# Performance work log

Hardware: AMD Instinct MI355X
Metric: run time of the kernel (lower is better)

The kernel has to match this reference:

```python
import jax, jax.numpy as jnp
import numpy as np
from jax import lax

B = 8; DIM = 256; NH = 8; PATCH = 8; WS = 28; STRIDE = 8; PAD = 14; ORF = 2.0; IMG = 448


def conv2d(x, w, stride, pad, groups=1):
    return lax.conv_general_dilated(
        x, w, (stride, stride), [(pad, pad), (pad, pad)],
        dimension_numbers=('NCHW', 'OIHW', 'NCHW'), feature_group_count=groups)


def ln_ch(x, g, b):
    # LayerNormProxy: LayerNorm over channel dim of NCHW
    m = jnp.mean(x, 1, keepdims=True)
    v = jnp.mean((x - m) ** 2, 1, keepdims=True)
    return (x - m) * lax.rsqrt(v + 1e-5) * g[None, :, None, None] + b[None, :, None, None]


def bilinear_sample(x, grid):
    # x: (N,C,H,W); grid: (N,Hg,Wg,2) in (x,y) order, [-1,1], align_corners=True, zeros padding
    N, C, H, W = x.shape
    gx = (grid[..., 0] + 1.0) * 0.5 * (W - 1)
    gy = (grid[..., 1] + 1.0) * 0.5 * (H - 1)
    x0 = jnp.floor(gx); y0 = jnp.floor(gy)
    x1 = x0 + 1.0; y1 = y0 + 1.0
    wx1 = gx - x0; wx0 = 1.0 - wx1
    wy1 = gy - y0; wy0 = 1.0 - wy1
    xf = x.reshape(N, C, H * W)

    def corner(ix, iy, w):
        valid = (ix >= 0) & (ix <= W - 1) & (iy >= 0) & (iy <= H - 1)
        ii = (jnp.clip(iy, 0, H - 1) * W + jnp.clip(ix, 0, W - 1)).astype(jnp.int32).reshape(N, -1)
        vals = jax.vmap(lambda f, i: f[:, i])(xf, ii)  # (N,C,Hg*Wg)
        return vals * (w * valid).reshape(N, 1, -1)

    out = (corner(x0, y0, wx0 * wy0) + corner(x1, y0, wx1 * wy0)
           + corner(x0, y1, wx0 * wy1) + corner(x1, y1, wx1 * wy1))
    return out.reshape(N, C, grid.shape[1], grid.shape[2])


def setup_inputs() -> dict:
    key = jax.random.key(0)
    ks = jax.random.split(key, 12)
    s = 0.02
    CG = 64
    return {
        'x': jax.random.normal(ks[0], (B, 3, IMG, IMG), jnp.float32),
        'patch_w': jax.random.normal(ks[1], (DIM, 3, PATCH, PATCH), jnp.float32) * s,
        'patch_b': jnp.zeros((DIM,), jnp.float32),
        'ln1_g': jnp.ones((DIM,), jnp.float32),
        'ln1_b': jnp.zeros((DIM,), jnp.float32),
        'wq': jax.random.normal(ks[2], (DIM, DIM), jnp.float32) * s,
        'bq': jnp.zeros((DIM,), jnp.float32),
        'wk': jax.random.normal(ks[3], (DIM, DIM), jnp.float32) * s,
        'bk': jnp.zeros((DIM,), jnp.float32),
        'wv': jax.random.normal(ks[4], (DIM, DIM), jnp.float32) * s,
        'bv': jnp.zeros((DIM,), jnp.float32),
        'wo': jax.random.normal(ks[5], (DIM, DIM), jnp.float32) * s,
        'bo': jnp.zeros((DIM,), jnp.float32),
        'off_dw_w': jax.random.normal(ks[6], (CG, 1, WS, WS), jnp.float32) * s,
        'off_dw_b': jnp.zeros((CG,), jnp.float32),
        'off_ln_g': jnp.ones((CG,), jnp.float32),
        'off_ln_b': jnp.zeros((CG,), jnp.float32),
        'off_pw_w': jax.random.normal(ks[7], (2, CG), jnp.float32) * s,
        'rpe_w1': jax.random.normal(ks[8], (32, 2), jnp.float32) * 0.1,
        'rpe_b1': jnp.zeros((32,), jnp.float32),
        'rpe_w2': jax.random.normal(ks[9], (2, 32), jnp.float32) * 0.1,
    }


def reference(x, patch_w, patch_b, ln1_g, ln1_b, wq, bq, wk, bk, wv, bv, wo, bo,
              off_dw_w, off_dw_b, off_ln_g, off_ln_b, off_pw_w, rpe_w1, rpe_b1, rpe_w2):
    Bn = x.shape[0]
    # patch embedding: Conv2d(3, dim, patch, patch) + LayerNormProxy
    feat = conv2d(x, patch_w, PATCH, 0) + patch_b[None, :, None, None]
    feat = ln_ch(feat, ln1_g, ln1_b)
    H, W = feat.shape[2], feat.shape[3]  # 56, 56
    G = (H // WS) * (W // WS)            # 4 groups
    CG = DIM // G; GH = NH // G; HC = DIM // NH
    # q projection (1x1 conv)
    q = jnp.einsum('oc,bchw->bohw', wq, feat) + bq[None, :, None, None]
    # offset network on per-group query features
    q_off = q.reshape(Bn * G, CG, H, W)
    off = conv2d(q_off, off_dw_w, STRIDE, PAD, groups=CG) + off_dw_b[None, :, None, None]
    off = jax.nn.gelu(ln_ch(off, off_ln_g, off_ln_b), approximate=False)
    off = jnp.einsum('oc,bchw->bohw', off_pw_w, off)   # (B*G, 2, Hk, Wk)
    Hk, Wk = off.shape[2], off.shape[3]
    ns = Hk * Wk
    rng = jnp.array([1.0 / (Hk - 1), 1.0 / (Wk - 1)], off.dtype).reshape(1, 2, 1, 1)
    offset = jnp.tanh(off) * rng * ORF
    offset = jnp.transpose(offset, (0, 2, 3, 1))  # (B*G, Hk, Wk, 2) in (y, x)
    # reference points, normalized to ~[-1, 1]
    ry = jnp.linspace(0.5, Hk - 0.5, Hk) / (Hk - 1) * 2.0 - 1.0
    rx = jnp.linspace(0.5, Wk - 0.5, Wk) / (Wk - 1) * 2.0 - 1.0
    ref = jnp.stack(jnp.meshgrid(ry, rx, indexing='ij'), -1)  # (Hk, Wk, 2)
    ref = jnp.broadcast_to(ref[None], (Bn * G, Hk, Wk, 2))
    pos = offset + ref
    # deformable sampling (grid expects (x, y) order)
    xs = bilinear_sample(feat.reshape(Bn * G, CG, H, W), pos[..., ::-1])  # (B*G, CG, Hk, Wk)
    xs = xs.reshape(Bn, DIM, ns)
    k = jnp.einsum('oc,bcn->bon', wk, xs) + bk[None, :, None]
    v = jnp.einsum('oc,bcn->bon', wv, xs) + bv[None, :, None]
    qh = q.reshape(Bn * NH, HC, H * W)
    kh = k.reshape(Bn * NH, HC, ns)
    vh = v.reshape(Bn * NH, HC, ns)
    attn = jnp.einsum('bcm,bcn->bmn', qh, kh) * (HC ** -0.5)  # (B*NH, HW, ns)
    # log-CPB relative position bias
    qy = jnp.linspace(0.0, float(H), H) / (H - 1) * 2.0 - 1.0
    qx = jnp.linspace(0.0, float(W), W) / (W - 1) * 2.0 - 1.0
    qg = jnp.stack(jnp.meshgrid(qy, qx, indexing='ij'), -1).reshape(H * W, 2)
    disp = (qg[None, :, None, :] - pos.reshape(Bn * G, ns, 2)[:, None, :, :]) * 4.0
    disp = jnp.sign(disp) * jnp.log2(jnp.abs(disp) + 1.0) / 3.0  # /log2(8)
    bias = jax.nn.relu(jnp.einsum('bmnc,hc->bmnh', disp, rpe_w1) + rpe_b1)
    bias = jnp.einsum('bmnh,oh->bmno', bias, rpe_w2)  # (B*G, HW, ns, GH)
    attn = attn + jnp.transpose(bias, (0, 3, 1, 2)).reshape(Bn * NH, H * W, ns)
    attn = jax.nn.softmax(attn, axis=-1)
    out = jnp.einsum('bmn,bcn->bcm', attn, vh).reshape(Bn, DIM, H, W)
    y = jnp.einsum('oc,bchw->bohw', wo, out) + bo[None, :, None, None]
    return (y, pos.reshape(Bn, G, Hk, Wk, 2), ref.reshape(Bn, G, Hk, Wk, 2))
```

## Files before the change

kernel.cpp:

```cpp
#include <hip/hip_runtime.h>
#include <hip/hip_fp16.h>
#include <cstddef>


typedef short bf16x8 __attribute__((ext_vector_type(8)));
typedef float f32x4 __attribute__((ext_vector_type(4)));

static __device__ __forceinline__ ushort f2bf(float f) {
  union { float f; unsigned u; } v; v.f = f;
  unsigned r = v.u + 0x7fffu + ((v.u >> 16) & 1u);
  return (ushort)(r >> 16);
}
static __device__ __forceinline__ float bf2f(ushort u) {
  union { unsigned u; float f; } v; v.u = ((unsigned)u) << 16;
  return v.f;
}
static __device__ __forceinline__ __half2 h2max(__half2 a, __half2 b) {
  return __halves2half2(__hmax(__low2half(a), __low2half(b)),
                        __hmax(__high2half(a), __high2half(b)));
}

#define OFF_FEATB 0u
#define OFF_QPK   3211264u
#define OFF_Q     6422528u
#define OFF_POS   12845056u
#define OFF_XS    12849152u
#define OFF_KPK   12980224u
#define OFF_VPK   13045760u
#define OFF_PWP   13111296u
#define OFF_WQP   13135872u
#define OFF_WOP   13168640u
#define OFF_WKP   13201408u
#define OFF_WVP   13234176u

__global__ __launch_bounds__(256) void k_xcvt(
    const float* __restrict__ x, ushort* __restrict__ xb) {
  const size_t i0 = ((size_t)blockIdx.x * 256 + threadIdx.x) * 8;
  float4 v0 = *(const float4*)(x + i0);
  float4 v1 = *(const float4*)(x + i0 + 4);
  bf16x8 o;
  o[0] = (short)f2bf(v0.x); o[1] = (short)f2bf(v0.y);
  o[2] = (short)f2bf(v0.z); o[3] = (short)f2bf(v0.w);
  o[4] = (short)f2bf(v1.x); o[5] = (short)f2bf(v1.y);
  o[6] = (short)f2bf(v1.z); o[7] = (short)f2bf(v1.w);
  *(bf16x8*)(xb + i0) = o;
}

__global__ __launch_bounds__(256) void k_pack(
    const float* __restrict__ pw, const float* __restrict__ wq,
    const float* __restrict__ wk, const float* __restrict__ wv,
    const float* __restrict__ wo, ushort* __restrict__ pwp,
    ushort* __restrict__ wqp, ushort* __restrict__ wkp,
    ushort* __restrict__ wvp, ushort* __restrict__ wop) {
  const int o = blockIdx.x, t = threadIdx.x, m = blockIdx.y;
  if (m == 0) {
    if (t < 192) pwp[((t >> 3) * 256 + o) * 8 + (t & 7)] = f2bf(pw[o * 192 + t]);
  } else {
    const float* in = (m == 1) ? wq : (m == 2) ? wk : (m == 3) ? wv : wo;
    ushort* out = (m == 1) ? wqp : (m == 2) ? wkp : (m == 3) ? wvp : wop;
    out[((t >> 3) * 256 + o) * 8 + (t & 7)] = f2bf(in[o * 256 + t]);
  }
}

__global__ __launch_bounds__(256) void k_patch_mfma(
    const ushort* __restrict__ xb, const ushort* __restrict__ pwp,
    const float* __restrict__ pb, const float* __restrict__ g1,
    const float* __restrict__ b1, ushort* __restrict__ featb) {
  __shared__ ushort Bs[2][8192];
  const int t = threadIdx.x;
  const int lane = t & 63, w = t >> 6;
  const int lr = lane & 15, kg = lane >> 4;
  const int m_base = blockIdx.x * 128 + w * 32;

  size_t abase[2];
#pragma unroll
  for (int mr = 0; mr < 2; mr++) {
    int mA = m_base + mr * 16 + lr;
    int bA = mA / 3136;
    int posA = mA - bA * 3136;
    int ohA = posA / 56;
    int owA = posA - ohA * 56;
    abase[mr] = (((size_t)bA * 3) * 448 + ohA * 8) * 448 + owA * 8;
  }

  f32x4 acc[2][16];
#pragma unroll
  for (int f = 0; f < 16; f++) {
    float bv = pb[f * 16 + lr];
    acc[0][f] = (f32x4){bv, bv, bv, bv};
    acc[1][f] = (f32x4){bv, bv, bv, bv};
  }

  bf16x8 st[4];
#pragma unroll
  for (int i = 0; i < 4; i++)
    st[i] = *(const bf16x8*)(pwp + i * 2048 + t * 8);
#pragma unroll
  for (int i = 0; i < 4; i++)
    *(bf16x8*)(&Bs[0][i * 2048 + t * 8]) = st[i];
  __syncthreads();
  int p = 0;
  for (int ks = 0; ks < 6; ks++) {
    if (ks < 5) {
#pragma unroll
      for (int i = 0; i < 4; i++)
        st[i] = *(const bf16x8*)(pwp + (ks + 1) * 8192 + i * 2048 + t * 8);
    }
    const int k8 = ks * 4 + kg;
    const int ci = k8 >> 3, ii = k8 & 7;
    bf16x8 a0 = *(const bf16x8*)(xb + abase[0] + (size_t)ci * 200704 + ii * 448);
    bf16x8 a1 = *(const bf16x8*)(xb + abase[1] + (size_t)ci * 200704 + ii * 448);
    const ushort* bsl = &Bs[p][kg * 2048];
#pragma unroll
    for (int f = 0; f < 16; f++) {
      bf16x8 bfr = *(const bf16x8*)(bsl + (f * 16 + lr) * 8);
      acc[0][f] = __builtin_amdgcn_mfma_f32_16x16x32_bf16(a0, bfr, acc[0][f], 0, 0, 0);
      acc[1][f] = __builtin_amdgcn_mfma_f32_16x16x32_bf16(a1, bfr, acc[1][f], 0, 0, 0);
    }
    __syncthreads();
    if (ks < 5) {
#pragma unroll
      for (int i = 0; i < 4; i++)
        *(bf16x8*)(&Bs[p ^ 1][i * 2048 + t * 8]) = st[i];
      __syncthreads();
      p ^= 1;
    }
  }

#pragma unroll
  for (int mr = 0; mr < 2; mr++) {
    float mean[4], rstd[4];
#pragma unroll
    for (int j = 0; j < 4; j++) {
      float s1 = 0.f, s2 = 0.f;
#pragma unroll
      for (int f = 0; f < 16; f++) { float v = acc[mr][f][j]; s1 += v; s2 += v * v; }
#pragma unroll
      for (int off = 8; off >= 1; off >>= 1) {
        s1 += __shfl_xor(s1, off);
        s2 += __shfl_xor(s2, off);
      }
      float mn = s1 * (1.f / 256.f);
      float var = s2 * (1.f / 256.f) - mn * mn;
      mean[j] = mn; rstd[j] = rsqrtf(var + 1e-5f);
    }
#pragma unroll
    for (int f = 0; f < 16; f++) {
      const int c = f * 16 + lr;
      const float gg = g1[c], bb = b1[c];
#pragma unroll
      for (int j = 0; j < 4; j++) {
        const int mo = m_base + mr * 16 + kg * 4 + j;
        float v = (acc[mr][f][j] - mean[j]) * rstd[j] * gg + bb;
        featb[(size_t)mo * 256 + c] = f2bf(v);
      }
    }
  }
}

__global__ __launch_bounds__(256) void k_gemm_mfma(
    const ushort* __restrict__ apk, const ushort* __restrict__ wp,
    const float* __restrict__ bias, float* __restrict__ out,
    ushort* __restrict__ opk) {
  __shared__ float smem[16448];
  ushort* Bs = (ushort*)smem;
  float* sA = smem;
  const int t = threadIdx.x;
  const int lane = t & 63, w = t >> 6;
  const int lr = lane & 15, kg = lane >> 4;
  const int m_base = blockIdx.x * 128 + w * 32;

  f32x4 acc[2][16];
#pragma unroll
  for (int f = 0; f < 16; f++) {
    float bv = bias[f * 16 + lr];
    acc[0][f] = (f32x4){bv, bv, bv, bv};
    acc[1][f] = (f32x4){bv, bv, bv, bv};
  }
  const ushort* a0p = apk + (size_t)(m_base + lr) * 256;
  const ushort* a1p = a0p + 16 * 256;

  bf16x8 st[4];
#pragma unroll
  for (int i = 0; i < 4; i++) st[i] = *(const bf16x8*)(wp + i * 2048 + t * 8);
#pragma unroll
  for (int i = 0; i < 4; i++) *(bf16x8*)(Bs + i * 2048 + t * 8) = st[i];
  __syncthreads();
  int p = 0;
  for (int ks = 0; ks < 8; ks++) {
    if (ks < 7) {
#pragma unroll
      for (int i = 0; i < 4; i++)
        st[i] = *(const bf16x8*)(wp + (ks + 1) * 8192 + i * 2048 + t * 8);
    }
    bf16x8 a0 = *(const bf16x8*)(a0p + ks * 32 + kg * 8);
    bf16x8 a1 = *(const bf16x8*)(a1p + ks * 32 + kg * 8);
    const ushort* bsl = Bs + p * 8192 + kg * 2048;
#pragma unroll
    for (int f = 0; f < 16; f++) {
      bf16x8 bfr = *(const bf16x8*)(bsl + (f * 16 + lr) * 8);
      acc[0][f] = __builtin_amdgcn_mfma_f32_16x16x32_bf16(a0, bfr, acc[0][f], 0, 0, 0);
      acc[1][f] = __builtin_amdgcn_mfma_f32_16x16x32_bf16(a1, bfr, acc[1][f], 0, 0, 0);
    }
    __syncthreads();
    if (ks < 7) {
#pragma unroll
      for (int i = 0; i < 4; i++)
        *(bf16x8*)(Bs + (p ^ 1) * 8192 + i * 2048 + t * 8) = st[i];
      __syncthreads();
      p ^= 1;
    }
  }
  __syncthreads();

#pragma unroll
  for (int h = 0; h < 2; h++) {
    if ((w >> 1) == h) {
      const int loc0 = (w & 1) * 32;
#pragma unroll
      for (int mr = 0; mr < 2; mr++)
#pragma unroll
        for (int f = 0; f < 16; f++)
#pragma unroll
          for (int j = 0; j < 4; j++)
            sA[(loc0 + mr * 16 + kg * 4 + j) * 257 + f * 16 + lr] = acc[mr][f][j];
    }
    __syncthreads();
    const int R0 = blockIdx.x * 128 + h * 64;
    const int bh = R0 / 3136;
    const int pos0 = R0 % 3136;
    {
      const int c = t;
      float* op = out + ((size_t)bh * 256 + c) * 3136 + pos0;
#pragma unroll
      for (int i4 = 0; i4 < 16; i4++) {
        float4 v;
        v.x = sA[(i4 * 4 + 0) * 257 + c];
        v.y = sA[(i4 * 4 + 1) * 257 + c];
        v.z = sA[(i4 * 4 + 2) * 257 + c];
        v.w = sA[(i4 * 4 + 3) * 257 + c];
        *(float4*)(op + i4 * 4) = v;
      }
    }
    if (opk) {
      const int mm = t & 63, cs = t >> 6;
      const int c0 = cs * 64;
#pragma unroll
      for (int jj = 0; jj < 8; jj++) {
        bf16x8 v8;
#pragma unroll
        for (int e = 0; e < 8; e++)
          v8[e] = (short)f2bf(sA[mm * 257 + c0 + jj * 8 + e]);
        *(bf16x8*)(opk + (size_t)(R0 + mm) * 256 + c0 + jj * 8) = v8;
      }
    }
    __syncthreads();
  }
}

__global__ __launch_bounds__(128) void k_offset_conv(
    const float* __restrict__ q, const float* __restrict__ dww,
    float* __restrict__ convo) {
  const int bg = blockIdx.y;
  const int wv = threadIdx.x >> 6;
  const int lane = threadIdx.x & 63;
  const int ch = blockIdx.x * 2 + wv;
  const int b = bg >> 2, g = bg & 3;

  __shared__ float pl[2][7072];
  float* P = pl[wv];
  for (int idx = lane; idx < 7072; idx += 64) P[idx] = 0.f;

  const float* qb = q + ((size_t)b * 256 + g * 64 + ch) * 3136;
  if (lane < 56) {
    for (int r = 0; r < 56; r++) {
      int hr = r + 14;
      P[hr * 84 + (lane + 14) + (hr >> 3)] = qb[r * 56 + lane];
    }
  }
  const int oh = lane >> 3, ow = lane & 7;
  const int chs = __builtin_amdgcn_readfirstlane(ch);
  const float* wr = dww + (size_t)chs * 784;
  float acc = 0.f;
  const int r0 = oh * 8, c0 = ow * 8;
  for (int i = 0; i < 28; i++) {
    int hr = r0 + i;
    const float* prow = P + hr * 84 + c0 + (hr >> 3);
    const float* wrr = wr + i * 28;
#pragma unroll
    for (int j = 0; j < 28; j++)
      acc = fmaf(prow[j], wrr[j], acc);
  }
  convo[bg * 4096 + lane * 64 + ch] = acc;
}

__global__ __launch_bounds__(256) void k_offset_post(
    const float* __restrict__ convo, const float* __restrict__ dwb,
    const float* __restrict__ lng, const float* __restrict__ lnb,
    const float* __restrict__ pww, float* __restrict__ pos_ws,
    float* __restrict__ out_pos, float* __restrict__ out_ref) {
  const int bg = blockIdx.y;
  const int wv = threadIdx.x >> 6;
  const int lane = threadIdx.x & 63;
  const int idx = blockIdx.x * 4 + wv;
  const int oh = idx >> 3, ow = idx & 7;

  float acc = convo[bg * 4096 + idx * 64 + lane] + dwb[lane];

  float s1 = acc, s2 = acc * acc;
#pragma unroll
  for (int off = 32; off >= 1; off >>= 1) {
    s1 += __shfl_xor(s1, off);
    s2 += __shfl_xor(s2, off);
  }
  float m = s1 * (1.f / 64.f);
  float var = s2 * (1.f / 64.f) - m * m;
  float val = (acc - m) * rsqrtf(var + 1e-5f) * lng[lane] + lnb[lane];
  val = 0.5f * val * (1.f + erff(val * 0.70710678118654752f));
  float p0 = pww[lane] * val, p1 = pww[64 + lane] * val;
#pragma unroll
  for (int off = 32; off >= 1; off >>= 1) {
    p0 += __shfl_xor(p0, off);
    p1 += __shfl_xor(p1, off);
  }
  if (lane == 0) {
    float offy = tanhf(p0) * (2.0f / 7.0f);
    float offx = tanhf(p1) * (2.0f / 7.0f);
    float ry = (0.5f + oh) * (2.0f / 7.0f) - 1.0f;
    float rx = (0.5f + ow) * (2.0f / 7.0f) - 1.0f;
    float py = offy + ry, px = offx + rx;
    int o = bg * 128 + idx * 2;
    pos_ws[o] = py;  pos_ws[o + 1] = px;
    out_pos[o] = py; out_pos[o + 1] = px;
    out_ref[o] = ry; out_ref[o + 1] = rx;
  }
}

__global__ __launch_bounds__(512) void k_sample_kv(
    const ushort* __restrict__ featb, const float* __restrict__ pos_ws,
    const ushort* __restrict__ wkp, const float* __restrict__ bk,
    const ushort* __restrict__ wvp, const float* __restrict__ bv,
    ushort* __restrict__ kpk, ushort* __restrict__ vpk) {
  const int b = blockIdx.x;
  const int t = threadIdx.x;
  __shared__ ushort xsb[64 * 264];
  __shared__ ushort Cst[2][64 * 264];

  {
    const int n = t >> 3, c0 = (t & 7) * 32;
    const int g = c0 >> 6;
    const int bg = b * 4 + g;
    float py = pos_ws[bg * 128 + n * 2];
    float px = pos_ws[bg * 128 + n * 2 + 1];
    float gx = (px + 1.f) * 27.5f;
    float gy = (py + 1.f) * 27.5f;
    float x0f = floorf(gx), y0f = floorf(gy);
    int x0 = (int)x0f, y0 = (int)y0f;
    float wx1 = gx - x0f, wx0 = 1.f - wx1;
    float wy1 = gy - y0f, wy0 = 1.f - wy1;
    float v00 = (x0 >= 0 && x0 <= 55 && y0 >= 0 && y0 <= 55) ? 1.f : 0.f;
    float v01 = (x0 + 1 >= 0 && x0 + 1 <= 55 && y0 >= 0 && y0 <= 55) ? 1.f : 0.f;
    float v10 = (x0 >= 0 && x0 <= 55 && y0 + 1 >= 0 && y0 + 1 <= 55) ? 1.f : 0.f;
    float v11 = (x0 + 1 >= 0 && x0 + 1 <= 55 && y0 + 1 >= 0 && y0 + 1 <= 55) ? 1.f : 0.f;
    float w00 = wx0 * wy0 * v00, w01 = wx1 * wy0 * v01;
    float w10 = wx0 * wy1 * v10, w11 = wx1 * wy1 * v11;
    int cx0 = min(max(x0, 0), 55), cx1 = min(max(x0 + 1, 0), 55);
    int cy0 = min(max(y0, 0), 55), cy1 = min(max(y0 + 1, 0), 55);
    const ushort* fb = featb + (size_t)b * 3136 * 256;
    const ushort* p00 = fb + (size_t)(cy0 * 56 + cx0) * 256;
    const ushort* p01 = fb + (size_t)(cy0 * 56 + cx1) * 256;
    const ushort* p10 = fb + (size_t)(cy1 * 56 + cx0) * 256;
    const ushort* p11 = fb + (size_t)(cy1 * 56 + cx1) * 256;
#pragma unroll
    for (int q4 = 0; q4 < 4; q4++) {
      const int c = c0 + q4 * 8;
      bf16x8 a00 = *(const bf16x8*)(p00 + c);
      bf16x8 a01 = *(const bf16x8*)(p01 + c);
      bf16x8 a10 = *(const bf16x8*)(p10 + c);
      bf16x8 a11 = *(const bf16x8*)(p11 + c);
      bf16x8 o8;
#pragma unroll
      for (int e = 0; e < 8; e++) {
        float s = bf2f((ushort)a00[e]) * w00 + bf2f((ushort)a01[e]) * w01 +
                  bf2f((ushort)a10[e]) * w10 + bf2f((ushort)a11[e]) * w11;
        o8[e] = (short)f2bf(s);
      }
      *(bf16x8*)(xsb + n * 264 + c) = o8;
    }
  }
  __syncthreads();

  const int lane = t & 63, w = t >> 6;
  const int mat = w >> 2, mt = w & 3;
  const int lr = lane & 15, kg = lane >> 4;
  const ushort* wp = mat ? wvp : wkp;
  const float* bs = mat ? bv : bk;
  f32x4 acc[16];
#pragma unroll
  for (int f = 0; f < 16; f++) {
    float bvv = bs[f * 16 + lr];
    acc[f] = (f32x4){bvv, bvv, bvv, bvv};
  }
#pragma unroll
  for (int ks = 0; ks < 8; ks++) {
    bf16x8 a = *(const bf16x8*)(xsb + (mt * 16 + lr) * 264 + ks * 32 + kg * 8);
#pragma unroll
    for (int f = 0; f < 16; f++) {
      bf16x8 bfr = *(const bf16x8*)(wp + (size_t)((ks * 4 + kg) * 256 + f * 16 + lr) * 8);
      acc[f] = __builtin_amdgcn_mfma_f32_16x16x32_bf16(a, bfr, acc[f], 0, 0, 0);
    }
  }
  ushort* cst = Cst[mat];
#pragma unroll
  for (int f = 0; f < 16; f++)
#pragma unroll
    for (int j = 0; j < 4; j++)
      cst[(mt * 16 + kg * 4 + j) * 264 + f * 16 + lr] = f2bf(acc[f][j]);
  __syncthreads();

#pragma unroll
  for (int pass = 0; pass < 4; pass++) {
    int grp = pass * 8 + (t >> 6);
    int h = grp >> 2, c8 = grp & 3, n2 = t & 63;
    bf16x8 v8 = *(const bf16x8*)(Cst[0] + n2 * 264 + h * 32 + c8 * 8);
    *(bf16x8*)(kpk + (size_t)(b * 8 + h) * 2048 + (c8 * 64 + n2) * 8) = v8;
  }
#pragma unroll
  for (int pass = 0; pass < 4; pass++) {
    int grp = pass * 512 + t;
    int h = grp >> 8, n8 = (grp >> 5) & 7, cc = grp & 31;
    bf16x8 v8;
#pragma unroll
    for (int e = 0; e < 8; e++)
      v8[e] = (short)Cst[1][(n8 * 8 + e) * 264 + h * 32 + cc];
    *(bf16x8*)(vpk + (size_t)(b * 8 + h) * 2048 + (n8 * 32 + cc) * 8) = v8;
  }
}

__global__ __launch_bounds__(256) void k_attn_mfma(
    const ushort* __restrict__ qpk, const ushort* __restrict__ kpk,
    const ushort* __restrict__ vpk, const float* __restrict__ pos_ws,
    const float* __restrict__ w1, const float* __restrict__ b1,
    const float* __restrict__ w2, ushort* __restrict__ attnpk) {
  const int bg = blockIdx.y;
  const int b = bg >> 2, g = bg & 3;
  const int m0 = blockIdx.x * 64;
  const int t = threadIdx.x;
  const int lane = t & 63, w = t >> 6;
  const int lr = lane & 15, kg = lane >> 4;

  __shared__ ushort Pbuf[4][16 * 72];
  __shared__ ushort outb[64 * 72];
  __shared__ float posl[128];
  __shared__ __half2 rpeh[32][6];

  if (t < 128) posl[t] = pos_ws[bg * 128 + t];
  if (t < 32) {
    rpeh[t][0] = __float2half2_rn(w1[t * 2]);
    rpeh[t][1] = __float2half2_rn(w1[t * 2 + 1]);
    rpeh[t][2] = __float2half2_rn(b1[t]);
    rpeh[t][3] = __float2half2_rn(w2[t]);
    rpeh[t][4] = __float2half2_rn(w2[32 + t]);
  }
  __syncthreads();

  float qgy[4], qgx[4];
#pragma unroll
  for (int j = 0; j < 4; j++) {
    int m = m0 + w * 16 + kg * 4 + j;
    int my = m / 56, mx = m % 56;
    qgy[j] = (float)my * (56.0f / 55.0f) * (2.0f / 55.0f) - 1.0f;
    qgx[j] = (float)mx * (56.0f / 55.0f) * (2.0f / 55.0f) - 1.0f;
  }
  float tyv[16], txv[16];
#pragma unroll
  for (int nf = 0; nf < 4; nf++) {
    int n = nf * 16 + lr;
    float py = posl[2 * n], px = posl[2 * n + 1];
#pragma unroll
    for (int j = 0; j < 4; j++) {
      float dy = (qgy[j] - py) * 4.f;
      float dx = (qgx[j] - px) * 4.f;
      tyv[nf * 4 + j] = copysignf(__log2f(fabsf(dy) + 1.f) * (1.f / 3.f), dy);
      txv[nf * 4 + j] = copysignf(__log2f(fabsf(dx) + 1.f) * (1.f / 3.f), dx);
    }
  }
  __half2 ty2[8], tx2[8], bb02[8], bb12[8];
  const __half2 z2 = __float2half2_rn(0.f);
#pragma unroll
  for (int k = 0; k < 8; k++) {
    ty2[k] = __floats2half2_rn(tyv[2 * k], tyv[2 * k + 1]);
    tx2[k] = __floats2half2_rn(txv[2 * k], txv[2 * k + 1]);
    bb02[k] = z2; bb12[k] = z2;
  }
  for (int jj = 0; jj < 32; jj++) {
    __half2 hy = rpeh[jj][0], hx = rpeh[jj][1], hb = rpeh[jj][2];
    __half2 ha = rpeh[jj][3], hc = rpeh[jj][4];
#pragma unroll
    for (int k = 0; k < 8; k++) {
      __half2 h = __hfma2(hy, ty2[k], __hfma2(hx, tx2[k], hb));
      h = h2max(h, z2);
      bb02[k] = __hfma2(ha, h, bb02[k]);
      bb12[k] = __hfma2(hc, h, bb12[k]);
    }
  }
  float bb0[16], bb1[16];
#pragma unroll
  for (int k = 0; k < 8; k++) {
    float2 f0 = __half22float2(bb02[k]);
    float2 f1 = __half22float2(bb12[k]);
    bb0[2 * k] = f0.x; bb0[2 * k + 1] = f0.y;
    bb1[2 * k] = f1.x; bb1[2 * k + 1] = f1.y;
  }

  const int mrow = m0 + w * 16 + lr;
  const float scale = 0.17677669529663687f;
  ushort* pb = Pbuf[w];

  f32x4 oacc[2][2];
#pragma unroll
  for (int gh = 0; gh < 2; gh++)
#pragma unroll
    for (int cf = 0; cf < 2; cf++) oacc[gh][cf] = (f32x4){0.f, 0.f, 0.f, 0.f};

#pragma unroll
  for (int gh = 0; gh < 2; gh++) {
    bf16x8 a = *(const bf16x8*)(qpk +
        ((size_t)(b * 3136 + mrow) * 256 + g * 64 + gh * 32 + kg * 8));
    const ushort* kbase = kpk + (size_t)(b * 8 + g * 2 + gh) * 2048;
    f32x4 s[4];
#pragma unroll
    for (int nf = 0; nf < 4; nf++) {
      bf16x8 bfr = *(const bf16x8*)(kbase + (size_t)(kg * 64 + nf * 16 + lr) * 8);
      s[nf] = __builtin_amdgcn_mfma_f32_16x16x32_bf16(
          a, bfr, (f32x4){0.f, 0.f, 0.f, 0.f}, 0, 0, 0);
    }
#pragma unroll
    for (int nf = 0; nf < 4; nf++)
#pragma unroll
      for (int j = 0; j < 4; j++)
        s[nf][j] = fmaf(s[nf][j], scale,
                        gh ? bb1[nf * 4 + j] : bb0[nf * 4 + j]);
#pragma unroll
    for (int j = 0; j < 4; j++) {
      float m1 = fmaxf(fmaxf(s[0][j], s[1][j]), fmaxf(s[2][j], s[3][j]));
#pragma unroll
      for (int o = 8; o >= 1; o >>= 1) m1 = fmaxf(m1, __shfl_xor(m1, o));
      float ss = 0.f;
#pragma unroll
      for (int nf = 0; nf < 4; nf++) {
        float e = __expf(s[nf][j] - m1);
        s[nf][j] = e;
        ss += e;
      }
#pragma unroll
      for (int o = 8; o >= 1; o >>= 1) ss += __shfl_xor(ss, o);
      float inv = 1.f / ss;
#pragma unroll
      for (int nf = 0; nf < 4; nf++) s[nf][j] *= inv;
    }
#pragma unroll
    for (int nf = 0; nf < 4; nf++)
#pragma unroll
      for (int j = 0; j < 4; j++)
        pb[(kg * 4 + j) * 72 + nf * 16 + lr] = f2bf(s[nf][j]);
    const ushort* vbase = vpk + (size_t)(b * 8 + g * 2 + gh) * 2048;
#pragma unroll
    for (int ks = 0; ks < 2; ks++) {
      bf16x8 pa = *(const bf16x8*)(pb + lr * 72 + ks * 32 + kg * 8);
#pragma unroll
      for (int cf = 0; cf < 2; cf++) {
        bf16x8 vb = *(const bf16x8*)(vbase +
            (size_t)((ks * 4 + kg) * 32 + cf * 16 + lr) * 8);
        oacc[gh][cf] = __builtin_amdgcn_mfma_f32_16x16x32_bf16(
            pa, vb, oacc[gh][cf], 0, 0, 0);
      }
    }
  }

#pragma unroll
  for (int gh = 0; gh < 2; gh++)
#pragma unroll
    for (int cf = 0; cf < 2; cf++)
#pragma unroll
      for (int j = 0; j < 4; j++)
        outb[(w * 16 + kg * 4 + j) * 72 + gh * 32 + cf * 16 + lr] =
            f2bf(oacc[gh][cf][j]);
  __syncthreads();
#pragma unroll
  for (int r2 = 0; r2 < 2; r2++) {
    int row = (t >> 3) + r2 * 32;
    int chunk = t & 7;
    bf16x8 v8 = *(const bf16x8*)(outb + row * 72 + chunk * 8);
    *(bf16x8*)(attnpk +
               ((size_t)(b * 3136 + m0 + row) * 256 + g * 64 + chunk * 8)) = v8;
  }
}

extern "C" void kernel_launch(void* const* d_in, const int* in_sizes, int n_in,
                              void* d_out, int out_size, void* d_ws,
                              size_t ws_size, hipStream_t stream) {
  const float* x       = (const float*)d_in[0];
  const float* patch_w = (const float*)d_in[1];
  const float* patch_b = (const float*)d_in[2];
  const float* ln1_g   = (const float*)d_in[3];
  const float* ln1_b   = (const float*)d_in[4];
  const float* wq      = (const float*)d_in[5];
  const float* bq      = (const float*)d_in[6];
  const float* wk      = (const float*)d_in[7];
  const float* bk      = (const float*)d_in[8];
  const float* wv      = (const float*)d_in[9];
  const float* bv      = (const float*)d_in[10];
  const float* wo      = (const float*)d_in[11];
  const float* bo      = (const float*)d_in[12];
  const float* off_dw_w = (const float*)d_in[13];
  const float* off_dw_b = (const float*)d_in[14];
  const float* off_ln_g = (const float*)d_in[15];
  const float* off_ln_b = (const float*)d_in[16];
  const float* off_pw_w = (const float*)d_in[17];
  const float* rpe_w1  = (const float*)d_in[18];
  const float* rpe_b1  = (const float*)d_in[19];
  const float* rpe_w2  = (const float*)d_in[20];

  float* ws = (float*)d_ws;
  ushort* featb = (ushort*)(ws + OFF_FEATB);
  ushort* attnpk = featb;
  ushort* qpk = (ushort*)(ws + OFF_QPK);
  float* q    = ws + OFF_Q;
  ushort* xb  = (ushort*)(ws + OFF_Q);
  float* posw = ws + OFF_POS;
  float* convo = ws + OFF_XS;
  ushort* kpk = (ushort*)(ws + OFF_KPK);
  ushort* vpk = (ushort*)(ws + OFF_VPK);
  ushort* pwp = (ushort*)(ws + OFF_PWP);
  ushort* wqp = (ushort*)(ws + OFF_WQP);
  ushort* wop = (ushort*)(ws + OFF_WOP);
  ushort* wkp = (ushort*)(ws + OFF_WKP);
  ushort* wvp = (ushort*)(ws + OFF_WVP);

  float* y = (float*)d_out;
  float* out_pos = y + 6422528;
  float* out_ref = out_pos + 4096;

  hipLaunchKernelGGL(k_xcvt, dim3(2352), dim3(256), 0, stream, x, xb);
  hipLaunchKernelGGL(k_pack, dim3(256, 5), dim3(256), 0, stream,
                     patch_w, wq, wk, wv, wo, pwp, wqp, wkp, wvp, wop);
  hipLaunchKernelGGL(k_patch_mfma, dim3(196), dim3(256), 0, stream,
                     xb, pwp, patch_b, ln1_g, ln1_b, featb);
  hipLaunchKernelGGL(k_gemm_mfma, dim3(196), dim3(256), 0, stream,
                     featb, wqp, bq, q, qpk);
  hipLaunchKernelGGL(k_offset_conv, dim3(32, 32), dim3(128), 0, stream,
                     q, off_dw_w, convo);
  hipLaunchKernelGGL(k_offset_post, dim3(16, 32), dim3(256), 0, stream,
                     convo, off_dw_b, off_ln_g, off_ln_b, off_pw_w,
                     posw, out_pos, out_ref);
  hipLaunchKernelGGL(k_sample_kv, dim3(8), dim3(512), 0, stream,
                     featb, posw, wkp, bk, wvp, bv, kpk, vpk);
  hipLaunchKernelGGL(k_attn_mfma, dim3(49, 32), dim3(256), 0, stream,
                     qpk, kpk, vpk, posw, rpe_w1, rpe_b1, rpe_w2, attnpk);
  hipLaunchKernelGGL(k_gemm_mfma, dim3(196), dim3(256), 0, stream,
                     attnpk, wop, bo, y, (ushort*)nullptr);
}
```

Before: 279.5 us.

## Split KV projection across sample blocks in fp32 and switch RPE MLP to fp32

Result: faster. 249.7 us (-10.6%).

```diff
diff --git a/kernel.cpp b/kernel.cpp
--- a/kernel.cpp
+++ b/kernel.cpp
@@ -1,5 +1,4 @@
 #include <hip/hip_runtime.h>
-#include <hip/hip_fp16.h>
 #include <cstddef>
 
 
@@ -14,10 +13,6 @@
 static __device__ __forceinline__ float bf2f(ushort u) {
   union { unsigned u; float f; } v; v.u = ((unsigned)u) << 16;
   return v.f;
-}
-static __device__ __forceinline__ __half2 h2max(__half2 a, __half2 b) {
-  return __halves2half2(__hmax(__low2half(a), __low2half(b)),
-                        __hmax(__high2half(a), __high2half(b)));
 }
 
 #define OFF_FEATB 0u
@@ -30,8 +25,8 @@
 #define OFF_PWP   13111296u
 #define OFF_WQP   13135872u
 #define OFF_WOP   13168640u
-#define OFF_WKP   13201408u
-#define OFF_WVP   13234176u
+#define OFF_WKT   13201408u
+#define OFF_WVT   13266944u
 
 __global__ __launch_bounds__(256) void k_xcvt(
     const float* __restrict__ x, ushort* __restrict__ xb) {
@@ -50,15 +45,19 @@
     const float* __restrict__ pw, const float* __restrict__ wq,
     const float* __restrict__ wk, const float* __restrict__ wv,
     const float* __restrict__ wo, ushort* __restrict__ pwp,
-    ushort* __restrict__ wqp, ushort* __restrict__ wkp,
-    ushort* __restrict__ wvp, ushort* __restrict__ wop) {
+    ushort* __restrict__ wqp, ushort* __restrict__ wop,
+    float* __restrict__ wkT, float* __restrict__ wvT) {
   const int o = blockIdx.x, t = threadIdx.x, m = blockIdx.y;
   if (m == 0) {
     if (t < 192) pwp[((t >> 3) * 256 + o) * 8 + (t & 7)] = f2bf(pw[o * 192 + t]);
+  } else if (m == 1) {
+    wqp[((t >> 3) * 256 + o) * 8 + (t & 7)] = f2bf(wq[o * 256 + t]);
+  } else if (m == 2) {
+    wop[((t >> 3) * 256 + o) * 8 + (t & 7)] = f2bf(wo[o * 256 + t]);
+  } else if (m == 3) {
+    wkT[t * 256 + o] = wk[o * 256 + t];
   } else {
-    const float* in = (m == 1) ? wq : (m == 2) ? wk : (m == 3) ? wv : wo;
-    ushort* out = (m == 1) ? wqp : (m == 2) ? wkp : (m == 3) ? wvp : wop;
-    out[((t >> 3) * 256 + o) * 8 + (t & 7)] = f2bf(in[o * 256 + t]);
+    wvT[t * 256 + o] = wv[o * 256 + t];
   }
 }
 
@@ -336,20 +335,19 @@
   }
 }
 
-__global__ __launch_bounds__(512) void k_sample_kv(
+__global__ __launch_bounds__(256) void k_sample_kv(
     const ushort* __restrict__ featb, const float* __restrict__ pos_ws,
-    const ushort* __restrict__ wkp, const float* __restrict__ bk,
-    const ushort* __restrict__ wvp, const float* __restrict__ bv,
+    const float* __restrict__ wkT, const float* __restrict__ bk,
+    const float* __restrict__ wvT, const float* __restrict__ bv,
     ushort* __restrict__ kpk, ushort* __restrict__ vpk) {
-  const int b = blockIdx.x;
+  const int b = blockIdx.y;
+  const int n = blockIdx.x;
   const int t = threadIdx.x;
-  __shared__ ushort xsb[64 * 264];
-  __shared__ ushort Cst[2][64 * 264];
-
+  const int g = t >> 6, lane = t & 63;
+  const int bg = b * 4 + g;
+
+  __shared__ float sxs[256];
   {
-    const int n = t >> 3, c0 = (t & 7) * 32;
-    const int g = c0 >> 6;
-    const int bg = b * 4 + g;
     float py = pos_ws[bg * 128 + n * 2];
     float px = pos_ws[bg * 128 + n * 2 + 1];
     float gx = (px + 1.f) * 27.5f;
@@ -358,83 +356,31 @@
     int x0 = (int)x0f, y0 = (int)y0f;
     float wx1 = gx - x0f, wx0 = 1.f - wx1;
     float wy1 = gy - y0f, wy0 = 1.f - wy1;
-    float v00 = (x0 >= 0 && x0 <= 55 && y0 >= 0 && y0 <= 55) ? 1.f : 0.f;
-    float v01 = (x0 + 1 >= 0 && x0 + 1 <= 55 && y0 >= 0 && y0 <= 55) ? 1.f : 0.f;
-    float v10 = (x0 >= 0 && x0 <= 55 && y0 + 1 >= 0 && y0 + 1 <= 55) ? 1.f : 0.f;
-    float v11 = (x0 + 1 >= 0 && x0 + 1 <= 55 && y0 + 1 >= 0 && y0 + 1 <= 55) ? 1.f : 0.f;
-    float w00 = wx0 * wy0 * v00, w01 = wx1 * wy0 * v01;
-    float w10 = wx0 * wy1 * v10, w11 = wx1 * wy1 * v11;
-    int cx0 = min(max(x0, 0), 55), cx1 = min(max(x0 + 1, 0), 55);
-    int cy0 = min(max(y0, 0), 55), cy1 = min(max(y0 + 1, 0), 55);
-    const ushort* fb = featb + (size_t)b * 3136 * 256;
-    const ushort* p00 = fb + (size_t)(cy0 * 56 + cx0) * 256;
-    const ushort* p01 = fb + (size_t)(cy0 * 56 + cx1) * 256;
-    const ushort* p10 = fb + (size_t)(cy1 * 56 + cx0) * 256;
-    const ushort* p11 = fb + (size_t)(cy1 * 56 + cx1) * 256;
-#pragma unroll
-    for (int q4 = 0; q4 < 4; q4++) {
-      const int c = c0 + q4 * 8;
-      bf16x8 a00 = *(const bf16x8*)(p00 + c);
-      bf16x8 a01 = *(const bf16x8*)(p01 + c);
-      bf16x8 a10 = *(const bf16x8*)(p10 + c);
-      bf16x8 a11 = *(const bf16x8*)(p11 + c);
-      bf16x8 o8;
-#pragma unroll
-      for (int e = 0; e < 8; e++) {
-        float s = bf2f((ushort)a00[e]) * w00 + bf2f((ushort)a01[e]) * w01 +
-                  bf2f((ushort)a10[e]) * w10 + bf2f((ushort)a11[e]) * w11;
-        o8[e] = (short)f2bf(s);
-      }
-      *(bf16x8*)(xsb + n * 264 + c) = o8;
-    }
+    const size_t mb = (size_t)b * 3136;
+    const int cofs = g * 64 + lane;
+    float acc = 0.f;
+    if (x0 >= 0 && x0 <= 55 && y0 >= 0 && y0 <= 55)
+      acc = fmaf(bf2f(featb[(mb + y0 * 56 + x0) * 256 + cofs]), wx0 * wy0, acc);
+    if (x0 + 1 >= 0 && x0 + 1 <= 55 && y0 >= 0 && y0 <= 55)
+      acc = fmaf(bf2f(featb[(mb + y0 * 56 + x0 + 1) * 256 + cofs]), wx1 * wy0, acc);
+    if (x0 >= 0 && x0 <= 55 && y0 + 1 >= 0 && y0 + 1 <= 55)
+      acc = fmaf(bf2f(featb[(mb + (y0 + 1) * 56 + x0) * 256 + cofs]), wx0 * wy1, acc);
+    if (x0 + 1 >= 0 && x0 + 1 <= 55 && y0 + 1 >= 0 && y0 + 1 <= 55)
+      acc = fmaf(bf2f(featb[(mb + (y0 + 1) * 56 + x0 + 1) * 256 + cofs]), wx1 * wy1, acc);
+    sxs[g * 64 + lane] = acc;
   }
   __syncthreads();
 
-  const int lane = t & 63, w = t >> 6;
-  const int mat = w >> 2, mt = w & 3;
-  const int lr = lane & 15, kg = lane >> 4;
-  const ushort* wp = mat ? wvp : wkp;
-  const float* bs = mat ? bv : bk;
-  f32x4 acc[16];
-#pragma unroll
-  for (int f = 0; f < 16; f++) {
-    float bvv = bs[f * 16 + lr];
-    acc[f] = (f32x4){bvv, bvv, bvv, bvv};
-  }
-#pragma unroll
-  for (int ks = 0; ks < 8; ks++) {
-    bf16x8 a = *(const bf16x8*)(xsb + (mt * 16 + lr) * 264 + ks * 32 + kg * 8);
-#pragma unroll
-    for (int f = 0; f < 16; f++) {
-      bf16x8 bfr = *(const bf16x8*)(wp + (size_t)((ks * 4 + kg) * 256 + f * 16 + lr) * 8);
-      acc[f] = __builtin_amdgcn_mfma_f32_16x16x32_bf16(a, bfr, acc[f], 0, 0, 0);
-    }
-  }
-  ushort* cst = Cst[mat];
-#pragma unroll
-  for (int f = 0; f < 16; f++)
-#pragma unroll
-    for (int j = 0; j < 4; j++)
-      cst[(mt * 16 + kg * 4 + j) * 264 + f * 16 + lr] = f2bf(acc[f][j]);
-  __syncthreads();
-
-#pragma unroll
-  for (int pass = 0; pass < 4; pass++) {
-    int grp = pass * 8 + (t >> 6);
-    int h = grp >> 2, c8 = grp & 3, n2 = t & 63;
-    bf16x8 v8 = *(const bf16x8*)(Cst[0] + n2 * 264 + h * 32 + c8 * 8);
-    *(bf16x8*)(kpk + (size_t)(b * 8 + h) * 2048 + (c8 * 64 + n2) * 8) = v8;
-  }
-#pragma unroll
-  for (int pass = 0; pass < 4; pass++) {
-    int grp = pass * 512 + t;
-    int h = grp >> 8, n8 = (grp >> 5) & 7, cc = grp & 31;
-    bf16x8 v8;
-#pragma unroll
-    for (int e = 0; e < 8; e++)
-      v8[e] = (short)Cst[1][(n8 * 8 + e) * 264 + h * 32 + cc];
-    *(bf16x8*)(vpk + (size_t)(b * 8 + h) * 2048 + (n8 * 32 + cc) * 8) = v8;
-  }
+  float ak = bk[t], av = bv[t];
+  for (int c = 0; c < 256; c++) {
+    float xv = sxs[c];
+    ak = fmaf(wkT[c * 256 + t], xv, ak);
+    av = fmaf(wvT[c * 256 + t], xv, av);
+  }
+  const int h = t >> 5, cc = t & 31;
+  const size_t base = (size_t)(b * 8 + h) * 2048;
+  kpk[base + (size_t)((cc >> 3) * 64 + n) * 8 + (cc & 7)] = f2bf(ak);
+  vpk[base + (size_t)((n >> 3) * 32 + cc) * 8 + (n & 7)] = f2bf(av);
 }
 
 __global__ __launch_bounds__(256) void k_attn_mfma(
@@ -449,18 +395,16 @@
   const int lane = t & 63, w = t >> 6;
   const int lr = lane & 15, kg = lane >> 4;
 
-  __shared__ ushort Pbuf[4][16 * 72];
+  __shared__ ushort Pbuf[4][16 * 88];
   __shared__ ushort outb[64 * 72];
   __shared__ float posl[128];
-  __shared__ __half2 rpeh[32][6];
+  __shared__ float4 rpe4[32];
+  __shared__ float rpeB[32];
 
   if (t < 128) posl[t] = pos_ws[bg * 128 + t];
   if (t < 32) {
-    rpeh[t][0] = __float2half2_rn(w1[t * 2]);
-    rpeh[t][1] = __float2half2_rn(w1[t * 2 + 1]);
-    rpeh[t][2] = __float2half2_rn(b1[t]);
-    rpeh[t][3] = __float2half2_rn(w2[t]);
-    rpeh[t][4] = __float2half2_rn(w2[32 + t]);
+    rpe4[t] = make_float4(w1[t * 2], w1[t * 2 + 1], b1[t], w2[t]);
+    rpeB[t] = w2[32 + t];
   }
   __syncthreads();
 
@@ -485,32 +429,18 @@
       txv[nf * 4 + j] = copysignf(__log2f(fabsf(dx) + 1.f) * (1.f / 3.f), dx);
     }
   }
-  __half2 ty2[8], tx2[8], bb02[8], bb12[8];
-  const __half2 z2 = __float2half2_rn(0.f);
-#pragma unroll
-  for (int k = 0; k < 8; k++) {
-    ty2[k] = __floats2half2_rn(tyv[2 * k], tyv[2 * k + 1]);
-    tx2[k] = __floats2half2_rn(txv[2 * k], txv[2 * k + 1]);
-    bb02[k] = z2; bb12[k] = z2;
-  }
+  float bb0[16], bb1[16];
+#pragma unroll
+  for (int p = 0; p < 16; p++) { bb0[p] = 0.f; bb1[p] = 0.f; }
   for (int jj = 0; jj < 32; jj++) {
-    __half2 hy = rpeh[jj][0], hx = rpeh[jj][1], hb = rpeh[jj][2];
-    __half2 ha = rpeh[jj][3], hc = rpeh[jj][4];
-#pragma unroll
-    for (int k = 0; k < 8; k++) {
-      __half2 h = __hfma2(hy, ty2[k], __hfma2(hx, tx2[k], hb));
-      h = h2max(h, z2);
-      bb02[k] = __hfma2(ha, h, bb02[k]);
-      bb12[k] = __hfma2(hc, h, bb12[k]);
-    }
-  }
-  float bb0[16], bb1[16];
-#pragma unroll
-  for (int k = 0; k < 8; k++) {
-    float2 f0 = __half22float2(bb02[k]);
-    float2 f1 = __half22float2(bb12[k]);
-    bb0[2 * k] = f0.x; bb0[2 * k + 1] = f0.y;
-    bb1[2 * k] = f1.x; bb1[2 * k + 1] = f1.y;
+    float4 r = rpe4[jj];
+    float wb = rpeB[jj];
+#pragma unroll
+    for (int p = 0; p < 16; p++) {
+      float hv = fmaxf(fmaf(r.x, tyv[p], fmaf(r.y, txv[p], r.z)), 0.f);
+      bb0[p] = fmaf(r.w, hv, bb0[p]);
+      bb1[p] = fmaf(wb, hv, bb1[p]);
+    }
   }
 
   const int mrow = m0 + w * 16 + lr;
@@ -563,11 +493,11 @@
     for (int nf = 0; nf < 4; nf++)
 #pragma unroll
       for (int j = 0; j < 4; j++)
-        pb[(kg * 4 + j) * 72 + nf * 16 + lr] = f2bf(s[nf][j]);
+        pb[(kg * 4 + j) * 88 + nf * 16 + lr] = f2bf(s[nf][j]);
     const ushort* vbase = vpk + (size_t)(b * 8 + g * 2 + gh) * 2048;
 #pragma unroll
     for (int ks = 0; ks < 2; ks++) {
-      bf16x8 pa = *(const bf16x8*)(pb + lr * 72 + ks * 32 + kg * 8);
+      bf16x8 pa = *(const bf16x8*)(pb + lr * 88 + ks * 32 + kg * 8);
 #pragma unroll
       for (int cf = 0; cf < 2; cf++) {
         bf16x8 vb = *(const bf16x8*)(vbase +
@@ -635,8 +565,8 @@
   ushort* pwp = (ushort*)(ws + OFF_PWP);
   ushort* wqp = (ushort*)(ws + OFF_WQP);
   ushort* wop = (ushort*)(ws + OFF_WOP);
-  ushort* wkp = (ushort*)(ws + OFF_WKP);
-  ushort* wvp = (ushort*)(ws + OFF_WVP);
+  float* wkT  = ws + OFF_WKT;
+  float* wvT  = ws + OFF_WVT;
 
   float* y = (float*)d_out;
   float* out_pos = y + 6422528;
@@ -644,7 +574,7 @@
 
   hipLaunchKernelGGL(k_xcvt, dim3(2352), dim3(256), 0, stream, x, xb);
   hipLaunchKernelGGL(k_pack, dim3(256, 5), dim3(256), 0, stream,
-                     patch_w, wq, wk, wv, wo, pwp, wqp, wkp, wvp, wop);
+                     patch_w, wq, wk, wv, wo, pwp, wqp, wop, wkT, wvT);
   hipLaunchKernelGGL(k_patch_mfma, dim3(196), dim3(256), 0, stream,
                      xb, pwp, patch_b, ln1_g, ln1_b, featb);
   hipLaunchKernelGGL(k_gemm_mfma, dim3(196), dim3(256), 0, stream,
@@ -654,8 +584,8 @@
   hipLaunchKernelGGL(k_offset_post, dim3(16, 32), dim3(256), 0, stream,
                      convo, off_dw_b, off_ln_g, off_ln_b, off_pw_w,
                      posw, out_pos, out_ref);
-  hipLaunchKernelGGL(k_sample_kv, dim3(8), dim3(512), 0, stream,
-                     featb, posw, wkp, bk, wvp, bv, kpk, vpk);
+  hipLaunchKernelGGL(k_sample_kv, dim3(64, 8), dim3(256), 0, stream,
+                     featb, posw, wkT, bk, wvT, bv, kpk, vpk);
   hipLaunchKernelGGL(k_attn_mfma, dim3(49, 32), dim3(256), 0, stream,
                      qpk, kpk, vpk, posw, rpe_w1, rpe_b1, rpe_w2, attnpk);
   hipLaunchKernelGGL(k_gemm_mfma, dim3(196), dim3(256), 0, stream,
```
